# Optimization experiments

Hardware: AMD Instinct MI355X
Metric: run time of the kernel (lower is better)

Reference implementation:

```python
import jax, jax.numpy as jnp
import numpy as np

HEADS = 16

def setup_inputs() -> dict:
    key = jax.random.key(0)
    k1, k2, k3 = jax.random.split(key, 3)
    B, T, C = 4, 2048, 1024
    s = 0.02
    return {
        "x": jax.random.normal(k1, (B, T, C), dtype=jnp.float32),
        "W_qkv": jax.random.normal(k2, (C, 3 * C), dtype=jnp.float32) * s,
        "b_qkv": jnp.zeros((3 * C,), dtype=jnp.float32),
        "W_pr": jax.random.normal(k3, (C, C), dtype=jnp.float32) * s,
        "b_pr": jnp.zeros((C,), dtype=jnp.float32),
    }

def reference(x, W_qkv, b_qkv, W_pr, b_pr):
    B, T, C = x.shape
    H = HEADS
    hd = C // H
    qkv = x @ W_qkv + b_qkv                     # [B,T,3C]
    q, k, v = jnp.split(qkv, 3, axis=-1)
    # [B,T,C] -> [B,H,T,hd]
    q = q.reshape(B, T, H, hd).transpose(0, 2, 1, 3)
    k = k.reshape(B, T, H, hd).transpose(0, 2, 1, 3)
    v = v.reshape(B, T, H, hd).transpose(0, 2, 1, 3)
    att = jnp.einsum('bhqd,bhkd->bhqk', q, k) * (1.0 / jnp.sqrt(jnp.float32(hd)))
    causal = jnp.tril(jnp.ones((T, T), dtype=bool))
    att = jnp.where(causal[None, None, :, :], att, jnp.float32(-jnp.inf))
    att = jax.nn.softmax(att, axis=-1)
    y = jnp.einsum('bhqk,bhkd->bhqd', att, v)   # [B,H,T,hd]
    y = y.transpose(0, 2, 1, 3).reshape(B, T, C)  # merge heads
    return y @ W_pr + b_pr
```

## Files before the change

### kernel.cpp

```cpp
#include <hip/hip_runtime.h>


typedef __attribute__((ext_vector_type(8))) short bf16x8;
typedef __attribute__((ext_vector_type(4))) float f32x4;

#define MFMA16(a, b, c) __builtin_amdgcn_mfma_f32_16x16x32_bf16(a, b, c, 0, 0, 0)

#define QK_SCALE 0.1803368801111244f

__device__ __forceinline__ unsigned short f2bf(float f) {
    union { float f; unsigned u; } v; v.f = f;
    unsigned r = v.u + 0x7fffu + ((v.u >> 16) & 1u);
    return (unsigned short)(r >> 16);
}

typedef __attribute__((address_space(1))) const unsigned int guint;
typedef __attribute__((address_space(3))) unsigned int luint;
__device__ __forceinline__ void gload16(const void* g, void* l) {
    __builtin_amdgcn_global_load_lds((guint*)g, (luint*)l, 16, 0, 0);
}

__device__ __forceinline__ float exp2_hw(float x) {
    float y;
    asm("v_exp_f32 %0, %1" : "=v"(y) : "v"(x));
    return y;
}

__device__ __forceinline__ unsigned cvt_pk_bf16(float lo, float hi) {
    unsigned w;
    asm("v_cvt_pk_bf16_f32 %0, %1, %2" : "=v"(w) : "v"(lo), "v"(hi));
    return w;
}

__global__ __launch_bounds__(256) void k_prep(
    const float* __restrict__ x, unsigned short* __restrict__ xb,
    const float* __restrict__ Wqkv, unsigned short* __restrict__ Wqt,
    const float* __restrict__ Wpr, unsigned short* __restrict__ Wpt) {
    __shared__ unsigned short tile[32][33];
    const int b = blockIdx.x;
    if (b < 2048) {
#pragma unroll
        for (int u = 0; u < 4; ++u) {
            int i = (b * 4 + u) * 256 + threadIdx.x;
            float4 v = reinterpret_cast<const float4*>(x)[i];
            ushort4 o;
            o.x = f2bf(v.x); o.y = f2bf(v.y); o.z = f2bf(v.z); o.w = f2bf(v.w);
            reinterpret_cast<ushort4*>(xb)[i] = o;
        }
        return;
    }
    const float* W; unsigned short* Wt; int K, N, idx;
    if (b < 5120) { W = Wqkv; Wt = Wqt; K = 1024; N = 3072; idx = b - 2048; }
    else          { W = Wpr;  Wt = Wpt; K = 1024; N = 1024; idx = b - 5120; }
    const int nb = N / 32;
    const int bn = (idx % nb) * 32, bk = (idx / nb) * 32;
    int tx = threadIdx.x & 31, ty = threadIdx.x >> 5;
#pragma unroll
    for (int i = 0; i < 32; i += 8)
        tile[ty + i][tx] = f2bf(W[(size_t)(bk + ty + i) * N + bn + tx]);
    __syncthreads();
#pragma unroll
    for (int i = 0; i < 32; i += 8)
        Wt[(size_t)(bn + ty + i) * K + bk + tx] = tile[tx][ty + i];
}


__global__ __launch_bounds__(512, 2) void k_gemm_qkv(
    const unsigned short* __restrict__ A,
    const unsigned short* __restrict__ Bt,
    const float* __restrict__ bias,
    unsigned short* __restrict__ Qo,
    unsigned short* __restrict__ Ko,
    unsigned short* __restrict__ Vto)
{
    constexpr int K = 1024;
    __shared__ alignas(16) char smem[147456];
    const int tid = threadIdx.x;
    const int wave = tid >> 6, lane = tid & 63;
    const int wr = wave >> 2, wc = wave & 3;
    const int lrow = lane & 15, lkg = lane >> 4;
    const int bid = blockIdx.x;
    const int xcd = bid & 7, sq = bid >> 3;
    const int bm = (xcd * 8 + (sq & 7)) * 128;
    const int bn = (sq >> 3) * 256;

    const int scol = (((tid & 7) ^ ((tid >> 3) & 7)) << 3);
    const int r0 = tid >> 3;
    const unsigned short* gA[2];
    const unsigned short* gB[4];
#pragma unroll
    for (int i = 0; i < 2; ++i)
        gA[i] = A + (size_t)(bm + i * 64 + r0) * K + scol;
#pragma unroll
    for (int i = 0; i < 4; ++i)
        gB[i] = Bt + (size_t)(bn + i * 64 + r0) * K + scol;

    f32x4 acc[4][4] = {};

#define GSTAGE(kt_, slot_)                                          \
    do {                                                            \
        char* ba_ = smem + (slot_) * 49152;                         \
        gload16(gA[0] + (kt_), ba_ + tid * 16);                     \
        gload16(gA[1] + (kt_), ba_ + 8192 + tid * 16);              \
        gload16(gB[0] + (kt_), ba_ + 16384 + tid * 16);             \
        gload16(gB[1] + (kt_), ba_ + 24576 + tid * 16);             \
        gload16(gB[2] + (kt_), ba_ + 32768 + tid * 16);             \
        gload16(gB[3] + (kt_), ba_ + 40960 + tid * 16);             \
    } while (0)

    GSTAGE(0, 0);
    GSTAGE(64, 1);
    int cs = 0;
    for (int t = 0; t < 16; ++t) {
        if (t < 15) asm volatile("s_waitcnt vmcnt(6)" ::: "memory");
        else        asm volatile("s_waitcnt vmcnt(0)" ::: "memory");
        __builtin_amdgcn_s_barrier();
        __builtin_amdgcn_sched_barrier(0);
        if (t + 2 < 16) {
            int ns = cs + 2; if (ns >= 3) ns -= 3;
            GSTAGE((t + 2) * 64, ns);
        }

        const char* Ab = smem + cs * 49152;
        const char* Bb = Ab + 16384;
        bf16x8 af[4][2], bfr[4][2];
#pragma unroll
        for (int m = 0; m < 4; ++m) {
            int R = wr * 64 + m * 16 + lrow;
#pragma unroll
            for (int k = 0; k < 2; ++k)
                af[m][k] = *reinterpret_cast<const bf16x8*>(
                    Ab + R * 128 + (((k * 4 + lkg) ^ (R & 7)) << 4));
        }
#pragma unroll
        for (int n = 0; n < 4; ++n) {
            int R = wc * 64 + n * 16 + lrow;
#pragma unroll
            for (int k = 0; k < 2; ++k)
                bfr[n][k] = *reinterpret_cast<const bf16x8*>(
                    Bb + R * 128 + (((k * 4 + lkg) ^ (R & 7)) << 4));
        }
#pragma unroll
        for (int m = 0; m < 4; ++m)
#pragma unroll
            for (int n = 0; n < 4; ++n) {
                acc[m][n] = MFMA16(af[m][0], bfr[n][0], acc[m][n]);
                acc[m][n] = MFMA16(af[m][1], bfr[n][1], acc[m][n]);
            }
        ++cs; if (cs == 3) cs = 0;
    }
#undef GSTAGE
    __syncthreads();

    const int which = bn >> 10;
    const int h0 = (bn & 1023) >> 6;
    const int bq = bm >> 11;
    const int t0 = bm & 2047;
    const float qs = (which == 0) ? QK_SCALE : 1.0f;
    unsigned short* Ep = (unsigned short*)smem;

    if (which != 2) {
#pragma unroll
        for (int m = 0; m < 4; ++m) {
            int trow = wr * 64 + m * 16 + lkg * 4;
#pragma unroll
            for (int n = 0; n < 4; ++n) {
                int cl = wc * 64 + n * 16 + lrow;
                float bia = bias[bn + cl];
#pragma unroll
                for (int r = 0; r < 4; ++r)
                    Ep[(trow + r) * 258 + cl] = f2bf((acc[m][n][r] + bia) * qs);
            }
        }
        __syncthreads();
        const int chunk = tid & 31, rbase = tid >> 5;
        const int head = h0 + (chunk >> 3), d0 = (chunk & 7) * 8;
        unsigned short* dst = (which == 0 ? Qo : Ko) +
            (size_t)((bq * 16 + head) * 2048 + t0) * 64 + d0;
#pragma unroll
        for (int s = 0; s < 8; ++s) {
            int row = s * 16 + rbase;
            bf16x8 v = *reinterpret_cast<const bf16x8*>(&Ep[row * 258 + chunk * 8]);
            *reinterpret_cast<bf16x8*>(dst + (size_t)row * 64) = v;
        }
    } else {
#pragma unroll
        for (int m = 0; m < 4; ++m) {
            int tl0 = wr * 64 + m * 16 + lkg * 4;
#pragma unroll
            for (int n = 0; n < 4; ++n) {
                int cl = wc * 64 + n * 16 + lrow;
                float bia = bias[bn + cl];
#pragma unroll
                for (int r = 0; r < 4; ++r) {
                    int tl = tl0 + r;
                    int pt = (tl & 0x60) | ((tl & 15) << 1) | ((tl >> 4) & 1);
                    Ep[cl * 130 + pt] = f2bf(acc[m][n][r] + bia);
                }
            }
        }
        __syncthreads();
        const int chunkt = tid & 15, crow = tid >> 4;
#pragma unroll
        for (int s = 0; s < 8; ++s) {
            int cl = s * 32 + crow;
            bf16x8 v = *reinterpret_cast<const bf16x8*>(&Ep[cl * 130 + chunkt * 8]);
            int bh = bq * 16 + h0 + (cl >> 6);
            size_t addr = ((size_t)(bh * 64 + (cl & 63)) * 2048) + t0 + chunkt * 8;
            *reinterpret_cast<bf16x8*>(Vto + addr) = v;
        }
    }
}

__global__ __launch_bounds__(256, 2) void k_attn(
    const unsigned short* __restrict__ Q,
    const unsigned short* __restrict__ Kg,
    const unsigned short* __restrict__ Vt,
    unsigned short* __restrict__ Y)
{
    __shared__ alignas(16) unsigned short Ks[2][4096];
    __shared__ alignas(16) unsigned short Vs[2][4096];
    __shared__ unsigned int Pu[4][32][36];
    const int tid = threadIdx.x;
    const int wave = tid >> 6, lane = tid & 63;
    const int lrow = lane & 15, lkg = lane >> 4;
    const int bh = blockIdx.x & 63;
    const int s = (blockIdx.x >> 6) & 3;
    const int band = blockIdx.x >> 8;
    const int j = (band == 0) ? 15 - s : (band == 1) ? 8 + s : (band == 2) ? 7 - s : s;
    const int qt = 4 * j + wave;
    const int q0 = qt * 32;
    const int qmax = q0 + 31;
    const int nt = 2 * j + 2;
    const int b = bh >> 4, hh = bh & 15;

    const unsigned short* Qh = Q + (size_t)bh * 2048 * 64;
    const unsigned short* Kh = Kg + (size_t)bh * 2048 * 64;
    const unsigned short* Vh = Vt + (size_t)bh * 64 * 2048;

    const int srow = tid >> 3;
    const int swz = ((tid & 7) ^ (srow & 7)) << 3;
    const unsigned short* gK = Kh + (size_t)srow * 64 + swz;
    const unsigned short* gV = Vh + (size_t)srow * 2048 + swz;
    char* dK0 = (char*)&Ks[0][0] + tid * 16;
    char* dV0 = (char*)&Vs[0][0] + tid * 16;

    bf16x8 aq[2][2];
#pragma unroll
    for (int h = 0; h < 2; ++h)
#pragma unroll
        for (int ks = 0; ks < 2; ++ks)
            aq[h][ks] = *reinterpret_cast<const bf16x8*>(
                &Qh[(size_t)(q0 + h * 16 + lrow) * 64 + ks * 32 + lkg * 8]);

    const bf16x8 ONES = { (short)0x3F80, (short)0x3F80, (short)0x3F80, (short)0x3F80,
                          (short)0x3F80, (short)0x3F80, (short)0x3F80, (short)0x3F80 };

    f32x4 acc[2][4] = {};
    f32x4 accl[2] = {};

#define STAGE(kb_, bufn_)                                           \
    do {                                                            \
        const unsigned short* k0_ = gK + (kb_) * 64;                \
        const unsigned short* v0_ = gV + (kb_);                     \
        char* dk_ = dK0 + (bufn_) * 8192;                           \
        char* dv_ = dV0 + (bufn_) * 8192;                           \
        gload16(k0_, dk_);                                          \
        gload16(k0_ + 2048, dk_ + 4096);                            \
        gload16(v0_, dv_);                                          \
        gload16(v0_ + 65536, dv_ + 4096);                           \
    } while (0)

    STAGE(0, 0);
    int buf = 0;

    for (int t = 0; t < nt; ++t) {
        asm volatile("s_waitcnt vmcnt(0)" ::: "memory");
        __builtin_amdgcn_s_barrier();
        __builtin_amdgcn_sched_barrier(0);
        if (t + 1 < nt) STAGE((t + 1) * 64, buf ^ 1);

        const int kb = t * 64;
        if (kb <= qmax) {
            const char* kbase = (const char*)&Ks[buf][0];
            const char* vbase = (const char*)&Vs[buf][0];

            f32x4 s_[2][4] = {};
            __builtin_amdgcn_s_setprio(1);
#pragma unroll
            for (int sub = 0; sub < 4; ++sub) {
                int krow = sub * 16 + lrow;
                bf16x8 kf0 = *reinterpret_cast<const bf16x8*>(
                    kbase + krow * 128 + ((lkg ^ (krow & 7)) << 4));
                bf16x8 kf1 = *reinterpret_cast<const bf16x8*>(
                    kbase + krow * 128 + (((4 + lkg) ^ (krow & 7)) << 4));
                s_[0][sub] = MFMA16(aq[0][0], kf0, s_[0][sub]);
                s_[0][sub] = MFMA16(aq[0][1], kf1, s_[0][sub]);
                s_[1][sub] = MFMA16(aq[1][0], kf0, s_[1][sub]);
                s_[1][sub] = MFMA16(aq[1][1], kf1, s_[1][sub]);
            }
            __builtin_amdgcn_s_setprio(0);

            const bool need_mask = (kb + 64 > q0);
#pragma unroll
            for (int h = 0; h < 2; ++h)
#pragma unroll
                for (int sub = 0; sub < 4; ++sub)
#pragma unroll
                    for (int r = 0; r < 4; ++r) {
                        float v = s_[h][sub][r];
                        if (need_mask) {
                            int key = kb + sub * 16 + lrow;
                            int q = q0 + h * 16 + lkg * 4 + r;
                            v = (key <= q) ? v : -1e30f;
                        }
                        s_[h][sub][r] = exp2_hw(v);
                    }

#pragma unroll
            for (int h = 0; h < 2; ++h) {
                int prow = h * 16 + lkg * 4;
#pragma unroll
                for (int r = 0; r < 4; ++r) {
                    Pu[wave][prow + r][lrow]      = cvt_pk_bf16(s_[h][0][r], s_[h][1][r]);
                    Pu[wave][prow + r][16 + lrow] = cvt_pk_bf16(s_[h][2][r], s_[h][3][r]);
                }
            }

            bf16x8 pf[2][2];
#pragma unroll
            for (int h = 0; h < 2; ++h)
#pragma unroll
                for (int kc = 0; kc < 2; ++kc)
                    pf[h][kc] = *reinterpret_cast<const bf16x8*>(
                        &Pu[wave][h * 16 + lrow][kc * 16 + lkg * 4]);

            __builtin_amdgcn_s_setprio(1);
#pragma unroll
            for (int tt = 0; tt < 4; ++tt) {
                int vrow = tt * 16 + lrow;
                bf16x8 vf0 = *reinterpret_cast<const bf16x8*>(
                    vbase + vrow * 128 + ((lkg ^ (vrow & 7)) << 4));
                bf16x8 vf1 = *reinterpret_cast<const bf16x8*>(
                    vbase + vrow * 128 + (((4 + lkg) ^ (vrow & 7)) << 4));
                acc[0][tt] = MFMA16(pf[0][0], vf0, acc[0][tt]);
                acc[0][tt] = MFMA16(pf[0][1], vf1, acc[0][tt]);
                acc[1][tt] = MFMA16(pf[1][0], vf0, acc[1][tt]);
                acc[1][tt] = MFMA16(pf[1][1], vf1, acc[1][tt]);
            }
#pragma unroll
            for (int h = 0; h < 2; ++h) {
                accl[h] = MFMA16(pf[h][0], ONES, accl[h]);
                accl[h] = MFMA16(pf[h][1], ONES, accl[h]);
            }
            __builtin_amdgcn_s_setprio(0);
        }

        buf ^= 1;
    }
#undef STAGE

#pragma unroll
    for (int h = 0; h < 2; ++h) {
        float inv[4];
#pragma unroll
        for (int r = 0; r < 4; ++r)
            inv[r] = 1.0f / accl[h][r];
#pragma unroll
        for (int t = 0; t < 4; ++t)
#pragma unroll
            for (int r = 0; r < 4; ++r) {
                int q = q0 + h * 16 + lkg * 4 + r;
                size_t idx = ((size_t)b * 2048 + q) * 1024 + hh * 64 + t * 16 + lrow;
                Y[idx] = f2bf(acc[h][t][r] * inv[r]);
            }
    }
}

__global__ __launch_bounds__(512, 2) void k_gemm_proj(
    const unsigned short* __restrict__ A,
    const unsigned short* __restrict__ Bt,
    const float* __restrict__ bias,
    float* __restrict__ out)
{
    constexpr int K = 1024;
    __shared__ alignas(16) char smem[147456];
    const int tid = threadIdx.x;
    const int wave = tid >> 6, lane = tid & 63;
    const int wr = wave >> 2, wc = wave & 3;
    const int lrow = lane & 15, lkg = lane >> 4;
    const int bid = blockIdx.x;
    const int xcd = bid & 7, sq = bid >> 3;
    const int bm = (xcd * 8 + (sq & 7)) * 128;
    const int bn = (sq >> 3) * 256;

    const int scol = (((tid & 7) ^ ((tid >> 3) & 7)) << 3);
    const int r0 = tid >> 3;
    const unsigned short* gA[2];
    const unsigned short* gB[4];
#pragma unroll
    for (int i = 0; i < 2; ++i)
        gA[i] = A + (size_t)(bm + i * 64 + r0) * K + scol;
#pragma unroll
    for (int i = 0; i < 4; ++i)
        gB[i] = Bt + (size_t)(bn + i * 64 + r0) * K + scol;

    f32x4 acc[4][4] = {};

#define GSTAGE(kt_, slot_)                                          \
    do {                                                            \
        char* ba_ = smem + (slot_) * 49152;                         \
        gload16(gA[0] + (kt_), ba_ + tid * 16);                     \
        gload16(gA[1] + (kt_), ba_ + 8192 + tid * 16);              \
        gload16(gB[0] + (kt_), ba_ + 16384 + tid * 16);             \
        gload16(gB[1] + (kt_), ba_ + 24576 + tid * 16);             \
        gload16(gB[2] + (kt_), ba_ + 32768 + tid * 16);             \
        gload16(gB[3] + (kt_), ba_ + 40960 + tid * 16);             \
    } while (0)

    GSTAGE(0, 0);
    GSTAGE(64, 1);
    int cs = 0;
    for (int t = 0; t < 16; ++t) {
        if (t < 15) asm volatile("s_waitcnt vmcnt(6)" ::: "memory");
        else        asm volatile("s_waitcnt vmcnt(0)" ::: "memory");
        __builtin_amdgcn_s_barrier();
        __builtin_amdgcn_sched_barrier(0);
        if (t + 2 < 16) {
            int ns = cs + 2; if (ns >= 3) ns -= 3;
            GSTAGE((t + 2) * 64, ns);
        }

        const char* Ab = smem + cs * 49152;
        const char* Bb = Ab + 16384;
        bf16x8 af[4][2], bfr[4][2];
#pragma unroll
        for (int m = 0; m < 4; ++m) {
            int R = wr * 64 + m * 16 + lrow;
#pragma unroll
            for (int k = 0; k < 2; ++k)
                af[m][k] = *reinterpret_cast<const bf16x8*>(
                    Ab + R * 128 + (((k * 4 + lkg) ^ (R & 7)) << 4));
        }
#pragma unroll
        for (int n = 0; n < 4; ++n) {
            int R = wc * 64 + n * 16 + lrow;
#pragma unroll
            for (int k = 0; k < 2; ++k)
                bfr[n][k] = *reinterpret_cast<const bf16x8*>(
                    Bb + R * 128 + (((k * 4 + lkg) ^ (R & 7)) << 4));
        }
#pragma unroll
        for (int m = 0; m < 4; ++m)
#pragma unroll
            for (int n = 0; n < 4; ++n) {
                acc[m][n] = MFMA16(af[m][0], bfr[n][0], acc[m][n]);
                acc[m][n] = MFMA16(af[m][1], bfr[n][1], acc[m][n]);
            }
        ++cs; if (cs == 3) cs = 0;
    }
#undef GSTAGE
    __syncthreads();

    float* Ep2 = (float*)smem;
#pragma unroll
    for (int m = 0; m < 4; ++m) {
        int row0 = wr * 64 + m * 16 + lkg * 4;
#pragma unroll
        for (int n = 0; n < 4; ++n) {
            int cl = wc * 64 + n * 16 + lrow;
            float bia = bias[bn + cl];
#pragma unroll
            for (int r = 0; r < 4; ++r)
                Ep2[(row0 + r) * 257 + cl] = acc[m][n][r] + bia;
        }
    }
    __syncthreads();
    const int chunk = tid & 63, rbase = tid >> 6;
#pragma unroll
    for (int s = 0; s < 16; ++s) {
        int row = s * 8 + rbase;
        float4 v = *reinterpret_cast<const float4*>(&Ep2[row * 257 + chunk * 4]);
        *reinterpret_cast<float4*>(
            &out[(size_t)(bm + row) * 1024 + bn + chunk * 4]) = v;
    }
}

extern "C" void kernel_launch(void* const* d_in, const int* in_sizes, int n_in,
                              void* d_out, int out_size, void* d_ws, size_t ws_size,
                              hipStream_t stream) {
    const float* x    = (const float*)d_in[0];
    const float* Wqkv = (const float*)d_in[1];
    const float* bqkv = (const float*)d_in[2];
    const float* Wpr  = (const float*)d_in[3];
    const float* bpr  = (const float*)d_in[4];
    float* out = (float*)d_out;

    char* ws = (char*)d_ws;
    unsigned short* xb  = (unsigned short*)(ws);
    unsigned short* Wqt = (unsigned short*)(ws + 16777216);
    unsigned short* Wpt = (unsigned short*)(ws + 23068672);
    unsigned short* Qb  = (unsigned short*)(ws + 25165824);
    unsigned short* Kb  = (unsigned short*)(ws + 41943040);
    unsigned short* Vt  = (unsigned short*)(ws + 58720256);
    unsigned short* Y   = xb;

    k_prep<<<6144, 256, 0, stream>>>(x, xb, Wqkv, Wqt, Wpr, Wpt);
    k_gemm_qkv<<<768, 512, 0, stream>>>(xb, Wqt, bqkv, Qb, Kb, Vt);
    k_attn<<<1024, 256, 0, stream>>>(Qb, Kb, Vt, Y);
    k_gemm_proj<<<256, 512, 0, stream>>>(Y, Wpt, bpr, out);
}
```

Measured before the change: 155.2 us.

## Retile projection GEMM to 128x128 blocks with 256 threads and K=32 stages

```diff
diff --git a/kernel.cpp b/kernel.cpp
--- a/kernel.cpp
+++ b/kernel.cpp
@@ -30,6 +30,10 @@
     unsigned w;
     asm("v_cvt_pk_bf16_f32 %0, %1, %2" : "=v"(w) : "v"(lo), "v"(hi));
     return w;
+}
+
+__device__ __forceinline__ int swz_src_col(int off) {
+    return ((((off >> 4) & 3) ^ ((off >> 7) & 3)) << 3);
 }
 
 __global__ __launch_bounds__(256) void k_prep(
@@ -63,7 +67,6 @@
     for (int i = 0; i < 32; i += 8)
         Wt[(size_t)(bn + ty + i) * K + bk + tx] = tile[tx][ty + i];
 }
-
 
 __global__ __launch_bounds__(512, 2) void k_gemm_qkv(
     const unsigned short* __restrict__ A,
@@ -377,112 +380,102 @@
     }
 }
 
-__global__ __launch_bounds__(512, 2) void k_gemm_proj(
+__global__ __launch_bounds__(256, 2) void k_gemm_proj(
     const unsigned short* __restrict__ A,
     const unsigned short* __restrict__ Bt,
     const float* __restrict__ bias,
     float* __restrict__ out)
 {
     constexpr int K = 1024;
-    __shared__ alignas(16) char smem[147456];
+    __shared__ alignas(16) char smem[49152];
+    float* Ep2 = (float*)smem;
     const int tid = threadIdx.x;
     const int wave = tid >> 6, lane = tid & 63;
-    const int wr = wave >> 2, wc = wave & 3;
+    const int wr = wave >> 1, wc = wave & 1;
     const int lrow = lane & 15, lkg = lane >> 4;
     const int bid = blockIdx.x;
     const int xcd = bid & 7, sq = bid >> 3;
     const int bm = (xcd * 8 + (sq & 7)) * 128;
-    const int bn = (sq >> 3) * 256;
-
-    const int scol = (((tid & 7) ^ ((tid >> 3) & 7)) << 3);
-    const int r0 = tid >> 3;
-    const unsigned short* gA[2];
-    const unsigned short* gB[4];
-#pragma unroll
-    for (int i = 0; i < 2; ++i)
-        gA[i] = A + (size_t)(bm + i * 64 + r0) * K + scol;
-#pragma unroll
-    for (int i = 0; i < 4; ++i)
-        gB[i] = Bt + (size_t)(bn + i * 64 + r0) * K + scol;
+    const int bn = (sq >> 3) * 128;
+
+    const int off0 = tid * 16, off1 = off0 + 4096;
+    const unsigned short* gA0 = A + (size_t)(bm + (off0 >> 6)) * K + swz_src_col(off0);
+    const unsigned short* gA1 = A + (size_t)(bm + (off1 >> 6)) * K + swz_src_col(off1);
+    const unsigned short* gB0 = Bt + (size_t)(bn + (off0 >> 6)) * K + swz_src_col(off0);
+    const unsigned short* gB1 = Bt + (size_t)(bn + (off1 >> 6)) * K + swz_src_col(off1);
 
     f32x4 acc[4][4] = {};
 
 #define GSTAGE(kt_, slot_)                                          \
     do {                                                            \
-        char* ba_ = smem + (slot_) * 49152;                         \
-        gload16(gA[0] + (kt_), ba_ + tid * 16);                     \
-        gload16(gA[1] + (kt_), ba_ + 8192 + tid * 16);              \
-        gload16(gB[0] + (kt_), ba_ + 16384 + tid * 16);             \
-        gload16(gB[1] + (kt_), ba_ + 24576 + tid * 16);             \
-        gload16(gB[2] + (kt_), ba_ + 32768 + tid * 16);             \
-        gload16(gB[3] + (kt_), ba_ + 40960 + tid * 16);             \
+        char* ba_ = smem + (slot_) * 16384;                         \
+        gload16(gA0 + (kt_), ba_ + off0);                           \
+        gload16(gA1 + (kt_), ba_ + off1);                           \
+        gload16(gB0 + (kt_), ba_ + 8192 + off0);                    \
+        gload16(gB1 + (kt_), ba_ + 8192 + off1);                    \
     } while (0)
 
     GSTAGE(0, 0);
-    GSTAGE(64, 1);
+    GSTAGE(32, 1);
     int cs = 0;
-    for (int t = 0; t < 16; ++t) {
-        if (t < 15) asm volatile("s_waitcnt vmcnt(6)" ::: "memory");
+    for (int t = 0; t < 32; ++t) {
+        if (t < 31) asm volatile("s_waitcnt vmcnt(4)" ::: "memory");
         else        asm volatile("s_waitcnt vmcnt(0)" ::: "memory");
         __builtin_amdgcn_s_barrier();
         __builtin_amdgcn_sched_barrier(0);
-        if (t + 2 < 16) {
+        if (t + 2 < 32) {
             int ns = cs + 2; if (ns >= 3) ns -= 3;
-            GSTAGE((t + 2) * 64, ns);
-        }
-
-        const char* Ab = smem + cs * 49152;
-        const char* Bb = Ab + 16384;
-        bf16x8 af[4][2], bfr[4][2];
+            GSTAGE((t + 2) * 32, ns);
+        }
+
+        const char* Asb = smem + cs * 16384;
+        const char* Bsb = Asb + 8192;
+        bf16x8 af[4], bfr[4];
 #pragma unroll
         for (int m = 0; m < 4; ++m) {
             int R = wr * 64 + m * 16 + lrow;
-#pragma unroll
-            for (int k = 0; k < 2; ++k)
-                af[m][k] = *reinterpret_cast<const bf16x8*>(
-                    Ab + R * 128 + (((k * 4 + lkg) ^ (R & 7)) << 4));
+            af[m] = *reinterpret_cast<const bf16x8*>(
+                Asb + R * 64 + ((lkg ^ ((R >> 1) & 3)) << 4));
         }
 #pragma unroll
         for (int n = 0; n < 4; ++n) {
             int R = wc * 64 + n * 16 + lrow;
-#pragma unroll
-            for (int k = 0; k < 2; ++k)
-                bfr[n][k] = *reinterpret_cast<const bf16x8*>(
-                    Bb + R * 128 + (((k * 4 + lkg) ^ (R & 7)) << 4));
+            bfr[n] = *reinterpret_cast<const bf16x8*>(
+                Bsb + R * 64 + ((lkg ^ ((R >> 1) & 3)) << 4));
         }
 #pragma unroll
         for (int m = 0; m < 4; ++m)
 #pragma unroll
-            for (int n = 0; n < 4; ++n) {
-                acc[m][n] = MFMA16(af[m][0], bfr[n][0], acc[m][n]);
-                acc[m][n] = MFMA16(af[m][1], bfr[n][1], acc[m][n]);
-            }
+            for (int n = 0; n < 4; ++n)
+                acc[m][n] = MFMA16(af[m], bfr[n], acc[m][n]);
         ++cs; if (cs == 3) cs = 0;
     }
 #undef GSTAGE
-    __syncthreads();
-
-    float* Ep2 = (float*)smem;
-#pragma unroll
-    for (int m = 0; m < 4; ++m) {
-        int row0 = wr * 64 + m * 16 + lkg * 4;
-#pragma unroll
-        for (int n = 0; n < 4; ++n) {
-            int cl = wc * 64 + n * 16 + lrow;
-            float bia = bias[bn + cl];
-#pragma unroll
-            for (int r = 0; r < 4; ++r)
-                Ep2[(row0 + r) * 257 + cl] = acc[m][n][r] + bia;
-        }
-    }
-    __syncthreads();
-    const int chunk = tid & 63, rbase = tid >> 6;
-#pragma unroll
-    for (int s = 0; s < 16; ++s) {
-        int row = s * 8 + rbase;
-        float4 v = *reinterpret_cast<const float4*>(&Ep2[row * 257 + chunk * 4]);
-        *reinterpret_cast<float4*>(
-            &out[(size_t)(bm + row) * 1024 + bn + chunk * 4]) = v;
+
+    const int chunk = tid >> 3;
+    const int r8 = tid & 7;
+#pragma unroll
+    for (int p = 0; p < 2; ++p) {
+        __syncthreads();
+        if (wr == p) {
+#pragma unroll
+            for (int m = 0; m < 4; ++m)
+#pragma unroll
+                for (int n = 0; n < 4; ++n) {
+                    int cl = wc * 64 + n * 16 + lrow;
+                    float bia = bias[bn + cl];
+#pragma unroll
+                    for (int r = 0; r < 4; ++r)
+                        Ep2[(m * 16 + lkg * 4 + r) * 129 + cl] = acc[m][n][r] + bia;
+                }
+        }
+        __syncthreads();
+#pragma unroll
+        for (int s = 0; s < 8; ++s) {
+            int row = r8 * 8 + s;
+            float4 v = *reinterpret_cast<const float4*>(&Ep2[row * 129 + chunk * 4]);
+            *reinterpret_cast<float4*>(&out[(size_t)(bm + p * 64 + row) * 1024 + bn + chunk * 4]) = v;
+        }
     }
 }
 
@@ -508,5 +501,5 @@
     k_prep<<<6144, 256, 0, stream>>>(x, xb, Wqkv, Wqt, Wpr, Wpt);
     k_gemm_qkv<<<768, 512, 0, stream>>>(xb, Wqt, bqkv, Qb, Kb, Vt);
     k_attn<<<1024, 256, 0, stream>>>(Qb, Kb, Vt, Y);
-    k_gemm_proj<<<256, 512, 0, stream>>>(Y, Wpt, bpr, out);
-}
+    k_gemm_proj<<<512, 256, 0, stream>>>(Y, Wpt, bpr, out);
+}
```

Result: slower. 160.5 us (+3.4%).
